# Kernel tuning notes

Hardware: AMD Instinct MI355X
Metric: run time of the kernel (lower is better)

## Reference

```python
import jax, jax.numpy as jnp
import numpy as np

P = 500000   # num optimizee params
H = 64       # hidden size
EPS = 1e-5

def _ln(x, g, b):
    # LayerNorm1D: unbiased std, eps added to std (matches torch .std())
    m = jnp.mean(x, axis=1, keepdims=True)
    s = jnp.std(x, axis=1, keepdims=True, ddof=1)
    return (x - m) / (s + EPS) * g + b

def _lstm_cell(x, hx, cx, Wi, bi, Wh, bh, gi, bgi, gh, bgh, gc, bc):
    z = _ln(x @ Wi.T + bi, gi, bgi) + _ln(hx @ Wh.T + bh, gh, bgh)  # [B,4H]
    i, f, o, g = jnp.split(z, 4, axis=1)
    cx = jax.nn.sigmoid(f) * cx + jax.nn.sigmoid(i) * jnp.tanh(g)
    hx = jax.nn.sigmoid(o) * jnp.tanh(_ln(cx, gc, bc))
    return hx, cx

def setup_inputs() -> dict:
    key = jax.random.key(0)
    ks = jax.random.split(key, 16)
    def n(k, shape, scale=0.05):
        return jax.random.normal(k, shape, dtype=jnp.float32) * scale
    ones = lambda s: jnp.ones(s, jnp.float32)
    zeros = lambda s: jnp.zeros(s, jnp.float32)
    inp = {
        'x': jax.random.normal(ks[0], (P,), dtype=jnp.float32),
        'W1': n(ks[1], (H, 1)), 'b1': zeros((H,)),
        'g1': ones((H,)), 'be1': zeros((H,)),
        'l0_Wi': n(ks[2], (4 * H, H)), 'l0_bi': zeros((4 * H,)),
        'l0_Wh': n(ks[3], (4 * H, H)), 'l0_bh': zeros((4 * H,)),
        'l0_gi': ones((4 * H,)), 'l0_bgi': zeros((4 * H,)),
        'l0_gh': ones((4 * H,)), 'l0_bgh': zeros((4 * H,)),
        'l0_gc': ones((H,)), 'l0_bc': zeros((H,)),
        'l1_Wi': n(ks[4], (4 * H, H)), 'l1_bi': zeros((4 * H,)),
        'l1_Wh': n(ks[5], (4 * H, H)), 'l1_bh': zeros((4 * H,)),
        'l1_gi': ones((4 * H,)), 'l1_bgi': zeros((4 * H,)),
        'l1_gh': ones((4 * H,)), 'l1_bgh': zeros((4 * H,)),
        'l1_gc': ones((H,)), 'l1_bc': zeros((H,)),
        'Wo': n(ks[6], (1, H)), 'bo': zeros((1,)),
    }
    return inp

def reference(x, W1, b1, g1, be1,
              l0_Wi, l0_bi, l0_Wh, l0_bh, l0_gi, l0_bgi, l0_gh, l0_bgh, l0_gc, l0_bc,
              l1_Wi, l1_bi, l1_Wh, l1_bh, l1_gi, l1_bgi, l1_gh, l1_bgh, l1_gc, l1_bc,
              Wo, bo):
    # AdaptiveMetaLearner.forward: append mean grad -> batch B = P+1
    xb = jnp.concatenate([x, jnp.mean(x)[None]])[:, None]        # [B,1]
    h = jnp.tanh(_ln(xb @ W1.T + b1, g1, be1))                    # [B,H]
    B = h.shape[0]
    hx = cx = jnp.zeros((B, H), h.dtype)
    hx, cx = _lstm_cell(h, hx, cx, l0_Wi, l0_bi, l0_Wh, l0_bh,
                        l0_gi, l0_bgi, l0_gh, l0_bgh, l0_gc, l0_bc)
    h2x = c2x = jnp.zeros((B, H), h.dtype)
    h2x, c2x = _lstm_cell(hx, h2x, c2x, l1_Wi, l1_bi, l1_Wh, l1_bh,
                          l1_gi, l1_bgi, l1_gh, l1_bgh, l1_gc, l1_bc)
    out = h2x @ Wo.T + bo                                         # [B,1]
    return out[:-1], out[-1:]                                     # (x_out [P,1], qt [1,1])
```

## Files before the change

kernel.cpp:

```cpp
#include <hip/hip_runtime.h>

#define EPS 1e-5f

typedef __attribute__((ext_vector_type(8))) short bf16x8;
typedef __attribute__((ext_vector_type(4))) short short4v;
typedef __attribute__((ext_vector_type(4))) float f32x4;

__device__ __forceinline__ float fexp(float x){ return __builtin_amdgcn_exp2f(x*1.4426950408889634f); }
__device__ __forceinline__ float frcp(float x){ return __builtin_amdgcn_rcpf(x); }
__device__ __forceinline__ float fsig(float x){ return frcp(1.0f + fexp(-x)); }
__device__ __forceinline__ float ftanh(float x){ return 1.0f - 2.0f*frcp(fexp(2.0f*x) + 1.0f); }

__device__ __forceinline__ short bfhi(float v){ return (short)(__float_as_uint(v) >> 16); }
__device__ __forceinline__ float bfhif(float v){ return __uint_as_float(__float_as_uint(v) & 0xFFFF0000u); }

__global__ void mean_part(const float* __restrict__ x, int P, float* __restrict__ part)
{
    __shared__ float red[256];
    int tid = blockIdx.x*256 + threadIdx.x;
    float s = 0.0f;
    for (int i = tid; i < P; i += 256*1024) s += x[i];
    red[threadIdx.x] = s; __syncthreads();
    for (int w = 128; w > 0; w >>= 1){
        if (threadIdx.x < w) red[threadIdx.x] += red[threadIdx.x + w];
        __syncthreads();
    }
    if (threadIdx.x == 0) part[blockIdx.x] = red[0];
}

__global__ void mean_fin(const float* __restrict__ part, float* __restrict__ ws, int P)
{
    __shared__ float red[1024];
    int t = threadIdx.x;
    red[t] = part[t]; __syncthreads();
    for (int w = 512; w > 0; w >>= 1){
        if (t < w) red[t] += red[t + w];
        __syncthreads();
    }
    if (t == 0) ws[0] = red[0] / (float)P;
}

__global__ void precomp_kernel(
    const float* __restrict__ bh0, const float* __restrict__ gh0,
    const float* __restrict__ bgh0, const float* __restrict__ bgi0,
    const float* __restrict__ bh1, const float* __restrict__ gh1,
    const float* __restrict__ bgh1, const float* __restrict__ bgi1,
    float* __restrict__ ws)
{
    const int l = blockIdx.x;
    const float* bh  = l ? bh1  : bh0;
    const float* gh  = l ? gh1  : gh0;
    const float* bgh = l ? bgh1 : bgh0;
    const float* bgi = l ? bgi1 : bgi0;
    float* add = ws + 1056 + l*256;
    int t = threadIdx.x;

    __shared__ float r1[256], r2[256];
    float v = bh[t];
    r1[t] = v; r2[t] = v*v; __syncthreads();
    for (int w = 128; w > 0; w >>= 1){
        if (t < w){ r1[t] += r1[t+w]; r2[t] += r2[t+w]; }
        __syncthreads();
    }
    float m   = r1[0] * (1.0f/256.0f);
    float var = (r2[0] - 256.0f*m*m) * (1.0f/255.0f);
    float s   = sqrtf(fmaxf(var, 0.0f));
    float c   = (v - m) * frcp(s + EPS) * gh[t] + bgh[t];
    add[t] = c + bgi[t];
}

__global__ __launch_bounds__(512, 2) void fwd_kernel(
    const float* __restrict__ x,
    const float* __restrict__ W1, const float* __restrict__ b1,
    const float* __restrict__ g1, const float* __restrict__ be1,
    const float* __restrict__ Wi0, const float* __restrict__ bi0,
    const float* __restrict__ gi0, const float* __restrict__ gc0, const float* __restrict__ bc0,
    const float* __restrict__ Wi1, const float* __restrict__ bi1,
    const float* __restrict__ gi1, const float* __restrict__ gc1, const float* __restrict__ bc1,
    const float* __restrict__ Wo, const float* __restrict__ bo,
    const float* __restrict__ ws, float* __restrict__ out, int P)
{
    __shared__ short wl[32768];
    __shared__ short hb[16384];

    const int tid  = threadIdx.x;
    const int wid  = tid >> 6;
    const int lane = tid & 63;
    const int c16  = lane & 15;
    const int q    = lane >> 4;
    const int row  = blockIdx.x*128 + wid*16 + c16;
    short* hbw = hb + wid*2048;
    const int swz = (c16 & 7) << 3;

    auto stage = [&](const float* __restrict__ W){
        #pragma unroll
        for (int i = 0; i < 8; ++i){
            int idx = i*512 + tid;
            int g = idx >> 4, k0 = (idx & 15) << 2;
            f32x4 w4 = *(const f32x4*)(W + (idx << 2));
            int si = ((g << 6) + k0) ^ ((g & 7) << 3);
            short4v hi = { bfhi(w4[0]), bfhi(w4[1]), bfhi(w4[2]), bfhi(w4[3]) };
            short4v lo = { bfhi(w4[0]-bfhif(w4[0])), bfhi(w4[1]-bfhif(w4[1])),
                           bfhi(w4[2]-bfhif(w4[2])), bfhi(w4[3]-bfhif(w4[3])) };
            *(short4v*)(wl + si)         = hi;
            *(short4v*)(wl + 16384 + si) = lo;
        }
    };

    stage(Wi0);

    float xv = 0.0f;
    if (row < P) xv = x[row];
    else if (row == P) xv = ws[0];

    {
        const int cb = q << 4;
        float h[16]; float sm = 0.f, sq = 0.f;
        #pragma unroll
        for (int j = 0; j < 16; ++j){
            float v = xv*W1[cb+j] + b1[cb+j];
            h[j] = v; sm += v; sq += v*v;
        }
        sm += __shfl_xor(sm, 16); sm += __shfl_xor(sm, 32);
        sq += __shfl_xor(sq, 16); sq += __shfl_xor(sq, 32);
        const float m   = sm * (1.0f/64.0f);
        const float var = (sq - 64.0f*m*m) * (1.0f/63.0f);
        const float inv = frcp(sqrtf(fmaxf(var, 0.0f)) + EPS);
        #pragma unroll
        for (int j = 0; j < 16; ++j)
            h[j] = ftanh((h[j]-m)*inv*g1[cb+j] + be1[cb+j]);
        #pragma unroll
        for (int j4 = 0; j4 < 4; ++j4){
            int si = ((c16 << 6) + cb + (j4 << 2)) ^ swz;
            short4v hi = { bfhi(h[j4*4+0]), bfhi(h[j4*4+1]), bfhi(h[j4*4+2]), bfhi(h[j4*4+3]) };
            short4v lo = { bfhi(h[j4*4+0]-bfhif(h[j4*4+0])), bfhi(h[j4*4+1]-bfhif(h[j4*4+1])),
                           bfhi(h[j4*4+2]-bfhif(h[j4*4+2])), bfhi(h[j4*4+3]-bfhif(h[j4*4+3])) };
            *(short4v*)(hbw + si)        = hi;
            *(short4v*)(hbw + 1024 + si) = lo;
        }
    }
    __syncthreads();

    float hout[16];

    auto do_layer = [&](const float* __restrict__ bi, const float* __restrict__ gi,
                        const float* __restrict__ addv, const float* __restrict__ gc,
                        const float* __restrict__ bc, bool writeback){
        bf16x8 bhh[2], bhl[2];
        #pragma unroll
        for (int ks = 0; ks < 2; ++ks){
            int si = ((c16 << 6) + ks*32 + (q << 3)) ^ swz;
            bhh[ks] = *(const bf16x8*)(hbw + si);
            bhl[ks] = *(const bf16x8*)(hbw + 1024 + si);
        }
        f32x4 acc[16];
        #pragma unroll
        for (int mt = 0; mt < 16; ++mt)
            acc[mt] = *(const f32x4*)(bi + mt*16 + (q << 2));
        #pragma unroll
        for (int mt = 0; mt < 16; ++mt){
            #pragma unroll
            for (int ks = 0; ks < 2; ++ks){
                int si = ((((mt << 4) + c16) << 6) + ks*32 + (q << 3)) ^ swz;
                bf16x8 whi = *(const bf16x8*)(wl + si);
                bf16x8 wlo = *(const bf16x8*)(wl + 16384 + si);
                acc[mt] = __builtin_amdgcn_mfma_f32_16x16x32_bf16(whi, bhh[ks], acc[mt], 0, 0, 0);
                acc[mt] = __builtin_amdgcn_mfma_f32_16x16x32_bf16(whi, bhl[ks], acc[mt], 0, 0, 0);
                acc[mt] = __builtin_amdgcn_mfma_f32_16x16x32_bf16(wlo, bhh[ks], acc[mt], 0, 0, 0);
            }
        }
        float sm = 0.f, sq = 0.f;
        #pragma unroll
        for (int mt = 0; mt < 16; ++mt){
            #pragma unroll
            for (int r = 0; r < 4; ++r){ float v = acc[mt][r]; sm += v; sq += v*v; }
        }
        sm += __shfl_xor(sm, 16); sm += __shfl_xor(sm, 32);
        sq += __shfl_xor(sq, 16); sq += __shfl_xor(sq, 32);
        const float m   = sm * (1.0f/256.0f);
        const float var = (sq - 256.0f*m*m) * (1.0f/255.0f);
        const float inv = frcp(sqrtf(fmaxf(var, 0.0f)) + EPS);

        float cx[16], oo[16];
        #pragma unroll
        for (int mt4 = 0; mt4 < 4; ++mt4){
            const f32x4 giI = *(const f32x4*)(gi   +       mt4*16 + (q << 2));
            const f32x4 giO = *(const f32x4*)(gi   + 128 + mt4*16 + (q << 2));
            const f32x4 giG = *(const f32x4*)(gi   + 192 + mt4*16 + (q << 2));
            const f32x4 adI = *(const f32x4*)(addv +       mt4*16 + (q << 2));
            const f32x4 adO = *(const f32x4*)(addv + 128 + mt4*16 + (q << 2));
            const f32x4 adG = *(const f32x4*)(addv + 192 + mt4*16 + (q << 2));
            #pragma unroll
            for (int r = 0; r < 4; ++r){
                const float i_ = (acc[mt4   ][r]-m)*inv*giI[r] + adI[r];
                const float o_ = (acc[mt4+ 8][r]-m)*inv*giO[r] + adO[r];
                const float g_ = (acc[mt4+12][r]-m)*inv*giG[r] + adG[r];
                cx[mt4*4+r] = fsig(i_) * ftanh(g_);
                oo[mt4*4+r] = o_;
            }
        }
        float s2 = 0.f, q2 = 0.f;
        #pragma unroll
        for (int t = 0; t < 16; ++t){ s2 += cx[t]; q2 += cx[t]*cx[t]; }
        s2 += __shfl_xor(s2, 16); s2 += __shfl_xor(s2, 32);
        q2 += __shfl_xor(q2, 16); q2 += __shfl_xor(q2, 32);
        const float mc = s2 * (1.0f/64.0f);
        const float vc = (q2 - 64.0f*mc*mc) * (1.0f/63.0f);
        const float ic = frcp(sqrtf(fmaxf(vc, 0.0f)) + EPS);
        #pragma unroll
        for (int mt4 = 0; mt4 < 4; ++mt4){
            const f32x4 gc4 = *(const f32x4*)(gc + mt4*16 + (q << 2));
            const f32x4 bc4 = *(const f32x4*)(bc + mt4*16 + (q << 2));
            #pragma unroll
            for (int r = 0; r < 4; ++r)
                hout[mt4*4+r] = fsig(oo[mt4*4+r]) * ftanh((cx[mt4*4+r]-mc)*ic*gc4[r] + bc4[r]);
        }
        if (writeback){
            #pragma unroll
            for (int mt4 = 0; mt4 < 4; ++mt4){
                int si = ((c16 << 6) + mt4*16 + (q << 2)) ^ swz;
                float a = hout[mt4*4+0], b = hout[mt4*4+1], c = hout[mt4*4+2], d = hout[mt4*4+3];
                short4v hi = { bfhi(a), bfhi(b), bfhi(c), bfhi(d) };
                short4v lo = { bfhi(a-bfhif(a)), bfhi(b-bfhif(b)), bfhi(c-bfhif(c)), bfhi(d-bfhif(d)) };
                *(short4v*)(hbw + si)        = hi;
                *(short4v*)(hbw + 1024 + si) = lo;
            }
        }
    };

    do_layer(bi0, gi0, ws + 1056, gc0, bc0, true);
    __syncthreads();
    stage(Wi1);
    __syncthreads();
    do_layer(bi1, gi1, ws + 1312, gc1, bc1, false);

    float o = 0.f;
    #pragma unroll
    for (int mt4 = 0; mt4 < 4; ++mt4){
        const f32x4 wo4 = *(const f32x4*)(Wo + mt4*16 + (q << 2));
        #pragma unroll
        for (int r = 0; r < 4; ++r) o += hout[mt4*4+r]*wo4[r];
    }
    o += __shfl_xor(o, 16); o += __shfl_xor(o, 32);
    if (q == 0 && row <= P) out[row] = o + bo[0];
}

extern "C" void kernel_launch(void* const* d_in, const int* in_sizes, int n_in,
                              void* d_out, int out_size, void* d_ws, size_t ws_size,
                              hipStream_t stream)
{
    (void)n_in; (void)out_size; (void)ws_size;
    const float* x     = (const float*)d_in[0];
    const float* W1    = (const float*)d_in[1];
    const float* b1    = (const float*)d_in[2];
    const float* g1    = (const float*)d_in[3];
    const float* be1   = (const float*)d_in[4];
    const float* l0_Wi = (const float*)d_in[5];
    const float* l0_bi = (const float*)d_in[6];
    const float* l0_bh = (const float*)d_in[8];
    const float* l0_gi = (const float*)d_in[9];
    const float* l0_bgi= (const float*)d_in[10];
    const float* l0_gh = (const float*)d_in[11];
    const float* l0_bgh= (const float*)d_in[12];
    const float* l0_gc = (const float*)d_in[13];
    const float* l0_bc = (const float*)d_in[14];
    const float* l1_Wi = (const float*)d_in[15];
    const float* l1_bi = (const float*)d_in[16];
    const float* l1_bh = (const float*)d_in[18];
    const float* l1_gi = (const float*)d_in[19];
    const float* l1_bgi= (const float*)d_in[20];
    const float* l1_gh = (const float*)d_in[21];
    const float* l1_bgh= (const float*)d_in[22];
    const float* l1_gc = (const float*)d_in[23];
    const float* l1_bc = (const float*)d_in[24];
    const float* Wo    = (const float*)d_in[25];
    const float* bo    = (const float*)d_in[26];

    int P = in_sizes[0];
    int B = P + 1;
    float* ws  = (float*)d_ws;
    float* out = (float*)d_out;

    mean_part<<<1024, 256, 0, stream>>>(x, P, ws + 16);
    mean_fin<<<1, 1024, 0, stream>>>(ws + 16, ws, P);
    precomp_kernel<<<2, 256, 0, stream>>>(
        l0_bh, l0_gh, l0_bgh, l0_bgi,
        l1_bh, l1_gh, l1_bgh, l1_bgi, ws);
    fwd_kernel<<<(B + 127)/128, 512, 0, stream>>>(
        x, W1, b1, g1, be1,
        l0_Wi, l0_bi, l0_gi, l0_gc, l0_bc,
        l1_Wi, l1_bi, l1_gi, l1_gc, l1_bc,
        Wo, bo, ws, out, P);
}
```

Before: 228.4 us.

## Stream low-half weight fragments from global memory to halve LDS and raise occupancy

Adds a precompute kernel that writes the bf16 low-residual of each LSTM input weight into workspace, already in MFMA fragment order. A new forward kernel keeps only the high bf16 half of the weights in LDS and reads the low half per lane from global/L2. This halves the weight LDS footprint and raises launch bounds from 2 to 4 blocks per CU, aiming for more overlap across the compute. In exchange it adds global loads inside the MFMA loop and a dependency on the workspace being large enough, with the old kernel kept as a fallback.

```diff
diff --git a/kernel.cpp b/kernel.cpp
--- a/kernel.cpp
+++ b/kernel.cpp
@@ -13,6 +13,8 @@
 
 __device__ __forceinline__ short bfhi(float v){ return (short)(__float_as_uint(v) >> 16); }
 __device__ __forceinline__ float bfhif(float v){ return __uint_as_float(__float_as_uint(v) & 0xFFFF0000u); }
+
+#define WS_NEED (2048*4 + 2*16384*2)
 
 __global__ void mean_part(const float* __restrict__ x, int P, float* __restrict__ part)
 {
@@ -40,7 +42,7 @@
     if (t == 0) ws[0] = red[0] / (float)P;
 }
 
-__global__ void precomp_kernel(
+__global__ void precomp_add(
     const float* __restrict__ bh0, const float* __restrict__ gh0,
     const float* __restrict__ bgh0, const float* __restrict__ bgi0,
     const float* __restrict__ bh1, const float* __restrict__ gh1,
@@ -69,7 +71,217 @@
     add[t] = c + bgi[t];
 }
 
-__global__ __launch_bounds__(512, 2) void fwd_kernel(
+__global__ void precomp_wlo(const float* __restrict__ Wi0, const float* __restrict__ Wi1,
+                            float* __restrict__ ws)
+{
+    const int l = blockIdx.x;
+    const float* Wi = l ? Wi1 : Wi0;
+    short* wlos = (short*)(ws + 2048) + l*16384;
+    int t = threadIdx.x;
+    for (int i = 0; i < 8; ++i){
+        int slot = i*256 + t;
+        int lane = slot & 63, mtks = slot >> 6;
+        int mt = mtks >> 1, ks = mtks & 1;
+        int g  = (mt << 4) + (lane & 15);
+        int k  = (ks << 5) + ((lane >> 4) << 3);
+        short tmp[8];
+        #pragma unroll
+        for (int j = 0; j < 8; ++j){
+            float w = Wi[(g << 6) + k + j];
+            tmp[j] = bfhi(w - bfhif(w));
+        }
+        short4v a = { tmp[0], tmp[1], tmp[2], tmp[3] };
+        short4v b = { tmp[4], tmp[5], tmp[6], tmp[7] };
+        *(short4v*)(wlos + slot*8)     = a;
+        *(short4v*)(wlos + slot*8 + 4) = b;
+    }
+}
+
+struct LayerParams { const float *bi, *gi, *addv, *gc, *bc; };
+
+__global__ __launch_bounds__(512, 4) void fwd_stream(
+    const float* __restrict__ x,
+    const float* __restrict__ W1, const float* __restrict__ b1,
+    const float* __restrict__ g1, const float* __restrict__ be1,
+    const float* __restrict__ Wi0, const float* __restrict__ bi0,
+    const float* __restrict__ gi0, const float* __restrict__ gc0, const float* __restrict__ bc0,
+    const float* __restrict__ Wi1, const float* __restrict__ bi1,
+    const float* __restrict__ gi1, const float* __restrict__ gc1, const float* __restrict__ bc1,
+    const float* __restrict__ Wo, const float* __restrict__ bo,
+    const float* __restrict__ ws, float* __restrict__ out, int P)
+{
+    __shared__ short wl[16384];
+    __shared__ short hb[16384];
+
+    const int tid  = threadIdx.x;
+    const int wid  = tid >> 6;
+    const int lane = tid & 63;
+    const int c16  = lane & 15;
+    const int q    = lane >> 4;
+    const int row  = blockIdx.x*128 + wid*16 + c16;
+    short* hbw = hb + wid*2048;
+    const int swz = (c16 & 7) << 3;
+    const short* SB = (const short*)(ws + 2048);
+
+    auto stage_hi = [&](const float* __restrict__ W){
+        #pragma unroll
+        for (int i = 0; i < 8; ++i){
+            int idx = i*512 + tid;
+            int g = idx >> 4, k0 = (idx & 15) << 2;
+            f32x4 w4 = *(const f32x4*)(W + (idx << 2));
+            int si = ((g << 6) + k0) ^ ((g & 7) << 3);
+            short4v hi = { bfhi(w4[0]), bfhi(w4[1]), bfhi(w4[2]), bfhi(w4[3]) };
+            *(short4v*)(wl + si) = hi;
+        }
+    };
+
+    stage_hi(Wi0);
+
+    float xv = 0.0f;
+    if (row < P) xv = x[row];
+    else if (row == P) xv = ws[0];
+
+    float h[16];
+    {
+        float sm = 0.f, sq = 0.f;
+        #pragma unroll
+        for (int mt4 = 0; mt4 < 4; ++mt4){
+            const f32x4 w14 = *(const f32x4*)(W1 + mt4*16 + (q << 2));
+            const f32x4 b14 = *(const f32x4*)(b1 + mt4*16 + (q << 2));
+            #pragma unroll
+            for (int r = 0; r < 4; ++r){
+                float v = xv*w14[r] + b14[r];
+                h[mt4*4+r] = v; sm += v; sq += v*v;
+            }
+        }
+        sm += __shfl_xor(sm, 16); sm += __shfl_xor(sm, 32);
+        sq += __shfl_xor(sq, 16); sq += __shfl_xor(sq, 32);
+        const float m   = sm * (1.0f/64.0f);
+        const float var = (sq - 64.0f*m*m) * (1.0f/63.0f);
+        const float inv = frcp(sqrtf(fmaxf(var, 0.0f)) + EPS);
+        #pragma unroll
+        for (int mt4 = 0; mt4 < 4; ++mt4){
+            const f32x4 g14  = *(const f32x4*)(g1  + mt4*16 + (q << 2));
+            const f32x4 be14 = *(const f32x4*)(be1 + mt4*16 + (q << 2));
+            #pragma unroll
+            for (int r = 0; r < 4; ++r)
+                h[mt4*4+r] = ftanh((h[mt4*4+r]-m)*inv*g14[r] + be14[r]);
+        }
+        #pragma unroll
+        for (int mt4 = 0; mt4 < 4; ++mt4){
+            int si = ((c16 << 6) + mt4*16 + (q << 2)) ^ swz;
+            float a = h[mt4*4+0], b = h[mt4*4+1], c = h[mt4*4+2], d = h[mt4*4+3];
+            short4v hi = { bfhi(a), bfhi(b), bfhi(c), bfhi(d) };
+            short4v lo = { bfhi(a-bfhif(a)), bfhi(b-bfhif(b)), bfhi(c-bfhif(c)), bfhi(d-bfhif(d)) };
+            *(short4v*)(hbw + si)        = hi;
+            *(short4v*)(hbw + 1024 + si) = lo;
+        }
+    }
+    __syncthreads();
+
+    float hout[16];
+
+    auto do_layer = [&](LayerParams p, const short* __restrict__ wlofrag, bool writeback){
+        bf16x8 bhh[2], bhl[2];
+        #pragma unroll
+        for (int ks = 0; ks < 2; ++ks){
+            int si = ((c16 << 6) + ks*32 + (q << 3)) ^ swz;
+            bhh[ks] = *(const bf16x8*)(hbw + si);
+            bhl[ks] = *(const bf16x8*)(hbw + 1024 + si);
+        }
+        f32x4 acc[16];
+        #pragma unroll
+        for (int mt = 0; mt < 16; ++mt)
+            acc[mt] = *(const f32x4*)(p.bi + mt*16 + (q << 2));
+        #pragma unroll
+        for (int mt = 0; mt < 16; ++mt){
+            #pragma unroll
+            for (int ks = 0; ks < 2; ++ks){
+                int si = ((((mt << 4) + c16) << 6) + ks*32 + (q << 3)) ^ swz;
+                bf16x8 whi = *(const bf16x8*)(wl + si);
+                bf16x8 wlo = *(const bf16x8*)(wlofrag + ((mt*2 + ks) << 9) + (lane << 3));
+                acc[mt] = __builtin_amdgcn_mfma_f32_16x16x32_bf16(whi, bhh[ks], acc[mt], 0, 0, 0);
+                acc[mt] = __builtin_amdgcn_mfma_f32_16x16x32_bf16(whi, bhl[ks], acc[mt], 0, 0, 0);
+                acc[mt] = __builtin_amdgcn_mfma_f32_16x16x32_bf16(wlo, bhh[ks], acc[mt], 0, 0, 0);
+            }
+        }
+        float sm = 0.f, sq = 0.f;
+        #pragma unroll
+        for (int mt = 0; mt < 16; ++mt){
+            #pragma unroll
+            for (int r = 0; r < 4; ++r){ float v = acc[mt][r]; sm += v; sq += v*v; }
+        }
+        sm += __shfl_xor(sm, 16); sm += __shfl_xor(sm, 32);
+        sq += __shfl_xor(sq, 16); sq += __shfl_xor(sq, 32);
+        const float m   = sm * (1.0f/256.0f);
+        const float var = (sq - 256.0f*m*m) * (1.0f/255.0f);
+        const float inv = frcp(sqrtf(fmaxf(var, 0.0f)) + EPS);
+
+        float cx[16], oo[16];
+        #pragma unroll
+        for (int mt4 = 0; mt4 < 4; ++mt4){
+            const f32x4 giI = *(const f32x4*)(p.gi   +       mt4*16 + (q << 2));
+            const f32x4 giO = *(const f32x4*)(p.gi   + 128 + mt4*16 + (q << 2));
+            const f32x4 giG = *(const f32x4*)(p.gi   + 192 + mt4*16 + (q << 2));
+            const f32x4 adI = *(const f32x4*)(p.addv +       mt4*16 + (q << 2));
+            const f32x4 adO = *(const f32x4*)(p.addv + 128 + mt4*16 + (q << 2));
+            const f32x4 adG = *(const f32x4*)(p.addv + 192 + mt4*16 + (q << 2));
+            #pragma unroll
+            for (int r = 0; r < 4; ++r){
+                const float i_ = (acc[mt4   ][r]-m)*inv*giI[r] + adI[r];
+                const float o_ = (acc[mt4+ 8][r]-m)*inv*giO[r] + adO[r];
+                const float g_ = (acc[mt4+12][r]-m)*inv*giG[r] + adG[r];
+                cx[mt4*4+r] = fsig(i_) * ftanh(g_);
+                oo[mt4*4+r] = o_;
+            }
+        }
+        float s2 = 0.f, q2 = 0.f;
+        #pragma unroll
+        for (int t = 0; t < 16; ++t){ s2 += cx[t]; q2 += cx[t]*cx[t]; }
+        s2 += __shfl_xor(s2, 16); s2 += __shfl_xor(s2, 32);
+        q2 += __shfl_xor(q2, 16); q2 += __shfl_xor(q2, 32);
+        const float mc = s2 * (1.0f/64.0f);
+        const float vc = (q2 - 64.0f*mc*mc) * (1.0f/63.0f);
+        const float ic = frcp(sqrtf(fmaxf(vc, 0.0f)) + EPS);
+        #pragma unroll
+        for (int mt4 = 0; mt4 < 4; ++mt4){
+            const f32x4 gc4 = *(const f32x4*)(p.gc + mt4*16 + (q << 2));
+            const f32x4 bc4 = *(const f32x4*)(p.bc + mt4*16 + (q << 2));
+            #pragma unroll
+            for (int r = 0; r < 4; ++r)
+                hout[mt4*4+r] = fsig(oo[mt4*4+r]) * ftanh((cx[mt4*4+r]-mc)*ic*gc4[r] + bc4[r]);
+        }
+        if (writeback){
+            #pragma unroll
+            for (int mt4 = 0; mt4 < 4; ++mt4){
+                int si = ((c16 << 6) + mt4*16 + (q << 2)) ^ swz;
+                float a = hout[mt4*4+0], b = hout[mt4*4+1], c = hout[mt4*4+2], d = hout[mt4*4+3];
+                short4v hi = { bfhi(a), bfhi(b), bfhi(c), bfhi(d) };
+                short4v lo = { bfhi(a-bfhif(a)), bfhi(b-bfhif(b)), bfhi(c-bfhif(c)), bfhi(d-bfhif(d)) };
+                *(short4v*)(hbw + si)        = hi;
+                *(short4v*)(hbw + 1024 + si) = lo;
+            }
+        }
+    };
+
+    do_layer({bi0, gi0, ws + 1056, gc0, bc0}, SB,          true);
+    __syncthreads();
+    stage_hi(Wi1);
+    __syncthreads();
+    do_layer({bi1, gi1, ws + 1312, gc1, bc1}, SB + 16384, false);
+
+    float o = 0.f;
+    #pragma unroll
+    for (int mt4 = 0; mt4 < 4; ++mt4){
+        const f32x4 wo4 = *(const f32x4*)(Wo + mt4*16 + (q << 2));
+        #pragma unroll
+        for (int r = 0; r < 4; ++r) o += hout[mt4*4+r]*wo4[r];
+    }
+    o += __shfl_xor(o, 16); o += __shfl_xor(o, 32);
+    if (q == 0 && row <= P) out[row] = o + bo[0];
+}
+
+__global__ __launch_bounds__(512, 2) void fwd_lds(
     const float* __restrict__ x,
     const float* __restrict__ W1, const float* __restrict__ b1,
     const float* __restrict__ g1, const float* __restrict__ be1,
@@ -143,9 +355,7 @@
 
     float hout[16];
 
-    auto do_layer = [&](const float* __restrict__ bi, const float* __restrict__ gi,
-                        const float* __restrict__ addv, const float* __restrict__ gc,
-                        const float* __restrict__ bc, bool writeback){
+    auto do_layer = [&](LayerParams p, bool writeback){
         bf16x8 bhh[2], bhl[2];
         #pragma unroll
         for (int ks = 0; ks < 2; ++ks){
@@ -156,7 +366,7 @@
         f32x4 acc[16];
         #pragma unroll
         for (int mt = 0; mt < 16; ++mt)
-            acc[mt] = *(const f32x4*)(bi + mt*16 + (q << 2));
+            acc[mt] = *(const f32x4*)(p.bi + mt*16 + (q << 2));
         #pragma unroll
         for (int mt = 0; mt < 16; ++mt){
             #pragma unroll
@@ -184,12 +394,12 @@
         float cx[16], oo[16];
         #pragma unroll
         for (int mt4 = 0; mt4 < 4; ++mt4){
-            const f32x4 giI = *(const f32x4*)(gi   +       mt4*16 + (q << 2));
-            const f32x4 giO = *(const f32x4*)(gi   + 128 + mt4*16 + (q << 2));
-            const f32x4 giG = *(const f32x4*)(gi   + 192 + mt4*16 + (q << 2));
-            const f32x4 adI = *(const f32x4*)(addv +       mt4*16 + (q << 2));
-            const f32x4 adO = *(const f32x4*)(addv + 128 + mt4*16 + (q << 2));
-            const f32x4 adG = *(const f32x4*)(addv + 192 + mt4*16 + (q << 2));
+            const f32x4 giI = *(const f32x4*)(p.gi   +       mt4*16 + (q << 2));
+            const f32x4 giO = *(const f32x4*)(p.gi   + 128 + mt4*16 + (q << 2));
+            const f32x4 giG = *(const f32x4*)(p.gi   + 192 + mt4*16 + (q << 2));
+            const f32x4 adI = *(const f32x4*)(p.addv +       mt4*16 + (q << 2));
+            const f32x4 adO = *(const f32x4*)(p.addv + 128 + mt4*16 + (q << 2));
+            const f32x4 adG = *(const f32x4*)(p.addv + 192 + mt4*16 + (q << 2));
             #pragma unroll
             for (int r = 0; r < 4; ++r){
                 const float i_ = (acc[mt4   ][r]-m)*inv*giI[r] + adI[r];
@@ -209,8 +419,8 @@
         const float ic = frcp(sqrtf(fmaxf(vc, 0.0f)) + EPS);
         #pragma unroll
         for (int mt4 = 0; mt4 < 4; ++mt4){
-            const f32x4 gc4 = *(const f32x4*)(gc + mt4*16 + (q << 2));
-            const f32x4 bc4 = *(const f32x4*)(bc + mt4*16 + (q << 2));
+            const f32x4 gc4 = *(const f32x4*)(p.gc + mt4*16 + (q << 2));
+            const f32x4 bc4 = *(const f32x4*)(p.bc + mt4*16 + (q << 2));
             #pragma unroll
             for (int r = 0; r < 4; ++r)
                 hout[mt4*4+r] = fsig(oo[mt4*4+r]) * ftanh((cx[mt4*4+r]-mc)*ic*gc4[r] + bc4[r]);
@@ -228,11 +438,11 @@
         }
     };
 
-    do_layer(bi0, gi0, ws + 1056, gc0, bc0, true);
+    do_layer({bi0, gi0, ws + 1056, gc0, bc0}, true);
     __syncthreads();
     stage(Wi1);
     __syncthreads();
-    do_layer(bi1, gi1, ws + 1312, gc1, bc1, false);
+    do_layer({bi1, gi1, ws + 1312, gc1, bc1}, false);
 
     float o = 0.f;
     #pragma unroll
@@ -249,7 +459,7 @@
                               void* d_out, int out_size, void* d_ws, size_t ws_size,
                               hipStream_t stream)
 {
-    (void)n_in; (void)out_size; (void)ws_size;
+    (void)n_in; (void)out_size;
     const float* x     = (const float*)d_in[0];
     const float* W1    = (const float*)d_in[1];
     const float* b1    = (const float*)d_in[2];
@@ -283,12 +493,22 @@
 
     mean_part<<<1024, 256, 0, stream>>>(x, P, ws + 16);
     mean_fin<<<1, 1024, 0, stream>>>(ws + 16, ws, P);
-    precomp_kernel<<<2, 256, 0, stream>>>(
+    precomp_add<<<2, 256, 0, stream>>>(
         l0_bh, l0_gh, l0_bgh, l0_bgi,
         l1_bh, l1_gh, l1_bgh, l1_bgi, ws);
-    fwd_kernel<<<(B + 127)/128, 512, 0, stream>>>(
-        x, W1, b1, g1, be1,
-        l0_Wi, l0_bi, l0_gi, l0_gc, l0_bc,
-        l1_Wi, l1_bi, l1_gi, l1_gc, l1_bc,
-        Wo, bo, ws, out, P);
-}
+
+    if (ws_size >= (size_t)WS_NEED){
+        precomp_wlo<<<2, 256, 0, stream>>>(l0_Wi, l1_Wi, ws);
+        fwd_stream<<<(B + 127)/128, 512, 0, stream>>>(
+            x, W1, b1, g1, be1,
+            l0_Wi, l0_bi, l0_gi, l0_gc, l0_bc,
+            l1_Wi, l1_bi, l1_gi, l1_gc, l1_bc,
+            Wo, bo, ws, out, P);
+    } else {
+        fwd_lds<<<(B + 127)/128, 512, 0, stream>>>(
+            x, W1, b1, g1, be1,
+            l0_Wi, l0_bi, l0_gi, l0_gc, l0_bc,
+            l1_Wi, l1_bi, l1_gi, l1_gc, l1_bc,
+            Wo, bo, ws, out, P);
+    }
+}
```

Measured after the change: 324.3 us. 1.42x slower.
